# Kernel optimization log

Hardware: AMD Instinct MI355X
Metric: run time of the kernel (lower is better)

The kernel has to match this reference:

```python
import jax, jax.numpy as jnp
import numpy as np

DIM = 256; CTX_DIM = 256; K = 7; SK = 5; NH = 4  # num_heads*2
HD = DIM // NH; SCALE = HD ** -0.5
H = 64; W = 64; HC = 56; WC = 56
LN_EPS = 1e-6; BN_EPS = 1e-5


def make_bias_idx(k, h, w):
    # Faithful port of ContMix.generate_idx + apply_rpb index construction.
    rs = 2 * k - 1
    idx_h = np.arange(k); idx_w = np.arange(k)
    idx_k = (idx_h[:, None] * rs + idx_w).reshape(-1)
    rep_h = np.ones(k, np.int64); rep_h[k // 2] = h - (k - 1)
    rep_w = np.ones(k, np.int64); rep_w[k // 2] = w - (k - 1)
    bias_hw = np.repeat(idx_h, rep_h)[:, None] * rs + np.repeat(idx_w, rep_w)  # (h, w)
    bias_idx = (bias_hw[..., None] + idx_k).reshape(-1, k * k)                 # (h*w, k^2)
    return jnp.asarray(bias_idx[::-1].copy())  # torch.flip along dim 0


def window_idx(n, k):
    # NATTEN-style clamped neighborhood window starts.
    s = np.clip(np.arange(n) - k // 2, 0, n - k)
    return jnp.asarray(s[:, None] + np.arange(k))  # (n, k)


BIDX1 = make_bias_idx(SK, H, W)
BIDX2 = make_bias_idx(K, H, W)
IDXI_S = window_idx(H, SK); IDXJ_S = window_idx(W, SK)
IDXI_L = window_idx(H, K);  IDXJ_L = window_idx(W, K)


def ln2d(x, g, b):
    # LayerNorm over channel dim per spatial location, x: (B, C, H, W)
    mu = x.mean(1, keepdims=True)
    var = ((x - mu) ** 2).mean(1, keepdims=True)
    return (x - mu) * jax.lax.rsqrt(var + LN_EPS) * g[None, :, None, None] + b[None, :, None, None]


def conv1x1(x, Wt):
    return jnp.einsum('oc,bchw->bohw', Wt, x)


def apply_rpb(attn, rpb, bias_idx, h, w):
    g = rpb.shape[0]
    r = rpb.reshape(g, -1)[:, bias_idx]  # (g, h*w, k^2)
    return attn + r.reshape(1, g, h, w, -1)


def na2d_av(attn, value, k, idx_i, idx_j):
    # attn: (B, G, H, W, k^2), value: (B, G, H, W, C)
    B, G, h, w, _ = attn.shape
    v = value[:, :, idx_i]        # (B, G, H, k, W, C)
    v = v[:, :, :, :, idx_j]      # (B, G, H, k, W, k, C)
    a = attn.reshape(B, G, h, w, k, k)
    return jnp.einsum('bghwpq,bghpwqc->bghwc', a, v)


def contmix_forward(x, ctx, Wq, gq, bq, Wk, gk, bk, Wproj, rpb1, rpb2, Wdy, bn_g, bn_b):
    B = x.shape[0]
    q = ln2d(conv1x1(x, Wq), gq, bq) * SCALE                       # (B, DIM, H, W)
    # AdaptiveAvgPool2d(7) on 56x56 -> exact 8x8 bins
    kctx = ctx.reshape(B, CTX_DIM, 7, HC // 7, 7, WC // 7).mean((3, 5))
    kf = ln2d(conv1x1(kctx, Wk), gk, bk)                            # (B, DIM, 7, 7)
    q = q.reshape(B, NH, HD, H * W)
    kf = kf.reshape(B, NH, HD, 49)
    wgt = jnp.einsum('bgcn,bgcl->bgnl', q, kf)                      # (B, 4, HW, 49)
    wgt = jnp.einsum('ml,bgnl->bgnm', Wproj, wgt)                   # (B, 4, HW, 74)
    wgt = wgt.reshape(B, NH, H, W, SK * SK + K * K)
    attn1 = wgt[:, :NH // 2, :, :, :SK * SK]                        # group1, 25
    attn2 = wgt[:, NH // 2:, :, :, SK * SK:]                        # group2, 49
    attn1 = jax.nn.softmax(apply_rpb(attn1, rpb1, BIDX1, H, W), -1)
    attn2 = jax.nn.softmax(apply_rpb(attn2, rpb2, BIDX2, H, W), -1)
    # 'b (m g c) h w -> m b g h w c', m=2, g=2
    v = x.reshape(B, 2, NH // 2, HD, H, W).transpose(1, 0, 2, 4, 5, 3)
    x1 = na2d_av(attn1, v[0], SK, IDXI_S, IDXJ_S)                   # (B, 2, H, W, HD)
    x2 = na2d_av(attn2, v[1], K, IDXI_L, IDXJ_L)
    out = jnp.concatenate([x1, x2], axis=1)                         # (B, 4, H, W, HD)
    out = out.transpose(0, 1, 4, 2, 3).reshape(B, DIM, H, W)
    out = conv1x1(out, Wdy)
    # BatchNorm2d in eval mode: running_mean=0, running_var=1
    out = out * (bn_g * jax.lax.rsqrt(jnp.float32(1.0) + BN_EPS))[None, :, None, None] + bn_b[None, :, None, None]
    return out


def setup_inputs() -> dict:
    key = jax.random.key(0)
    ks = jax.random.split(key, 10)
    d = {}
    d['x'] = jax.random.normal(ks[0], (4, DIM, H, W), jnp.float32)
    d['ctx'] = jax.random.normal(ks[1], (4, CTX_DIM, HC, WC), jnp.float32)
    d['Wq'] = jax.random.normal(ks[2], (DIM, DIM), jnp.float32) * 0.02
    d['gq'] = jnp.ones((DIM,), jnp.float32)
    d['bq'] = jnp.zeros((DIM,), jnp.float32)
    d['Wk'] = jax.random.normal(ks[3], (DIM, CTX_DIM), jnp.float32) * 0.02
    d['gk'] = jnp.ones((DIM,), jnp.float32)
    d['bk'] = jnp.zeros((DIM,), jnp.float32)
    d['Wproj'] = jax.random.normal(ks[4], (SK * SK + K * K, 49), jnp.float32) * 0.1
    d['rpb1'] = jax.random.normal(ks[5], (NH // 2, 2 * SK - 1, 2 * SK - 1), jnp.float32) * 0.02
    d['rpb2'] = jax.random.normal(ks[6], (NH // 2, 2 * K - 1, 2 * K - 1), jnp.float32) * 0.02
    d['Wdy'] = jax.random.normal(ks[7], (DIM, DIM), jnp.float32) * 0.02
    d['bn_g'] = jnp.ones((DIM,), jnp.float32)
    d['bn_b'] = jnp.zeros((DIM,), jnp.float32)
    return d


def reference(x, ctx, Wq, gq, bq, Wk, gk, bk, Wproj, rpb1, rpb2, Wdy, bn_g, bn_b):
    return contmix_forward(x, ctx, Wq, gq, bq, Wk, gk, bk, Wproj, rpb1, rpb2, Wdy, bn_g, bn_b)
```

## Files before the change

kernel.cpp:

```cpp
#include <hip/hip_runtime.h>

#define DEV __device__ __forceinline__

typedef __bf16 bf16x8 __attribute__((ext_vector_type(8)));
typedef __bf16 bf16x4 __attribute__((ext_vector_type(4)));
typedef float floatx4 __attribute__((ext_vector_type(4)));

__global__ __launch_bounds__(256)
void prep_kernel(const float* __restrict__ Wq, const float* __restrict__ Wdy,
                 const float* __restrict__ ctx, const float* __restrict__ x,
                 __bf16* __restrict__ wqb, __bf16* __restrict__ wdyb,
                 float* __restrict__ kctx, __bf16* __restrict__ xt) {
  __shared__ float tile[64][65];
  int bid = blockIdx.x, t = threadIdx.x;
  if (bid < 256) {
    int i = bid * 256 + t;
    wqb[i]  = (__bf16)Wq[i];
    wdyb[i] = (__bf16)Wdy[i];
  } else if (bid < 512) {
    int bc = (bid - 256) * 4 + (t >> 6);
    const float* src = ctx + (size_t)bc * (56 * 56);
    int w = t & 63;
#pragma unroll
    for (int pi = 0; pi < 7; ++pi) {
      float s = 0.f;
      if (w < 56) {
#pragma unroll
        for (int di = 0; di < 8; ++di) s += src[(pi * 8 + di) * 56 + w];
      }
      s += __shfl_down(s, 4);
      s += __shfl_down(s, 2);
      s += __shfl_down(s, 1);
      if (w < 56 && (w & 7) == 0)
        kctx[(size_t)bc * 49 + pi * 7 + (w >> 3)] = s * (1.f / 64.f);
    }
  } else {
    int idx = bid - 512;
    int b = idx >> 8, c0 = ((idx >> 6) & 3) * 64, n0 = (idx & 63) * 64;
    int lane = t & 63, rg = t >> 6;
    const float* src = x + ((size_t)b * 256 + c0) * 4096 + n0;
    for (int i = rg; i < 64; i += 4) tile[i][lane] = src[(size_t)i * 4096 + lane];
    __syncthreads();
    __bf16* dst = xt + ((size_t)b * 4096 + n0) * 256 + c0;
    for (int i = rg; i < 64; i += 4) dst[(size_t)i * 256 + lane] = (__bf16)tile[lane][i];
  }
}

__global__ __launch_bounds__(256)
void kf_ln_kernel(const float* __restrict__ kctx, const float* __restrict__ Wk,
                  const float* __restrict__ gk, const float* __restrict__ bk,
                  float* __restrict__ kf) {
  int b = blockIdx.x / 49, l = blockIdx.x % 49;
  __shared__ float xs[256];
  __shared__ float r1[4], r2[4];
  int o = threadIdx.x;
  xs[o] = kctx[((size_t)b * 256 + o) * 49 + l];
  __syncthreads();
  const float* wrow = Wk + (size_t)o * 256;
  float acc = 0.f;
#pragma unroll 8
  for (int c = 0; c < 256; c += 4) {
    float4 wv = *(const float4*)(wrow + c);
    acc += wv.x * xs[c] + wv.y * xs[c + 1] + wv.z * xs[c + 2] + wv.w * xs[c + 3];
  }
  float s1 = acc, s2 = acc * acc;
#pragma unroll
  for (int off = 32; off > 0; off >>= 1) {
    s1 += __shfl_down(s1, off);
    s2 += __shfl_down(s2, off);
  }
  int wv_ = o >> 6, ln = o & 63;
  if (ln == 0) { r1[wv_] = s1; r2[wv_] = s2; }
  __syncthreads();
  float mu  = (r1[0] + r1[1] + r1[2] + r1[3]) * (1.f / 256.f);
  float var = (r2[0] + r2[1] + r2[2] + r2[3]) * (1.f / 256.f) - mu * mu;
  float rstd = rsqrtf(var + 1e-6f);
  kf[((size_t)b * 256 + o) * 49 + l] = (acc - mu) * rstd * gk[o] + bk[o];
}

__global__ __launch_bounds__(256)
void kfp_kernel(const float* __restrict__ kf, const float* __restrict__ Wproj,
                __bf16* __restrict__ kfpT) {
  int bg = blockIdx.x; int b = bg >> 2, g = bg & 3;
  int m0 = blockIdx.y * 16;
  __shared__ float kfs[64][50];
  __shared__ float wps[16][50];
  int t = threadIdx.x;
  for (int i = t; i < 64 * 49; i += 256) {
    int d = i / 49, l = i % 49;
    kfs[d][l] = kf[((size_t)b * 256 + g * 64 + d) * 49 + l];
  }
  for (int i = t; i < 16 * 49; i += 256) {
    int m = i / 49, l = i % 49;
    wps[m][l] = (m0 + m < 74) ? Wproj[(m0 + m) * 49 + l] : 0.f;
  }
  __syncthreads();
  for (int i = t; i < 64 * 16; i += 256) {
    int d = i >> 4, m = i & 15;
    float s = 0.f;
    if (m0 + m < 74) {
#pragma unroll 7
      for (int l = 0; l < 49; ++l) s += kfs[d][l] * wps[m][l];
    }
    kfpT[(size_t)bg * 5120 + (m0 + m) * 64 + d] = (__bf16)s;
  }
}

DEV int rep_idx(int p, int kc, int t1, int sub) {
  return p < kc ? p : (p < t1 ? kc : p - sub);
}

template <int KK>
DEV void softmax_write(const float* wms, const float* rpb_s, __bf16* __restrict__ attnL,
                       int bg, int n_glob, int row) {
  constexpr int CNT = KK * KK;
  constexpr int RS  = 2 * KK - 1;
  constexpr int KC  = KK / 2;
  constexpr int T1  = KC + (64 - KK + 1);
  constexpr int SUB = 64 - KK;
  constexpr int MLO = (KK == 5) ? 0 : 25;
  constexpr int PW  = (KK == 5) ? 32 : 56;
  int h = n_glob >> 6, w = n_glob & 63;
  int rh = rep_idx(63 - h, KC, T1, SUB);
  int rw = rep_idx(63 - w, KC, T1, SUB);
  float vals[CNT];
  float mx = -1e30f;
#pragma unroll
  for (int m = 0; m < CNT; ++m) {
    int ki = m / KK, kj = m % KK;
    float v = wms[row * 81 + MLO + m] + rpb_s[(rh + ki) * RS + rw + kj];
    vals[m] = v; mx = fmaxf(mx, v);
  }
  float ssum = 0.f;
#pragma unroll
  for (int m = 0; m < CNT; ++m) { float e = __expf(vals[m] - mx); vals[m] = e; ssum += e; }
  float inv = 1.f / ssum;
  __bf16 hv[PW];
#pragma unroll
  for (int m = 0; m < PW; ++m) hv[m] = (__bf16)(m < CNT ? vals[m] * inv : 0.f);
  __bf16* ap = attnL + ((size_t)bg * 4096 + n_glob) * 56;
#pragma unroll
  for (int i = 0; i < PW / 8; ++i) *(bf16x8*)(ap + i * 8) = *(bf16x8*)&hv[i * 8];
}

__global__ __launch_bounds__(512, 1)
void qattn_kernel(const __bf16* __restrict__ Wb, const __bf16* __restrict__ XT,
                  const __bf16* __restrict__ kfpT,
                  const float* __restrict__ gq, const float* __restrict__ bq,
                  const float* __restrict__ rpb1, const float* __restrict__ rpb2,
                  __bf16* __restrict__ attnL) {
  __shared__ float wms[256 * 81];
  __shared__ float rpb_s[500];
  __shared__ float gqs[256], bqs[256];
  __shared__ float red_s[4][64], red_q[4][64];
  __shared__ float st_mu[64], st_rs[64];
  __bf16* As  = (__bf16*)wms;
  __bf16* Bs  = (__bf16*)wms + 256 * 72;
  __bf16* Aat = (__bf16*)wms;

  int b  = blockIdx.z;
  int n0 = blockIdx.x * 64;
  int t  = threadIdx.x;
  int lane = t & 63, wv = t >> 6;
  int oq = wv & 3, nh = wv >> 2;
  int col = lane & 15, quad = lane >> 4;

  if (t < 256) {
    gqs[t] = gq[t] * 0.125f;
    bqs[t] = bq[t] * 0.125f;
  }
  for (int i = t; i < 162; i += 512) rpb_s[i] = rpb1[i];
  for (int i = t; i < 338; i += 512) rpb_s[162 + i] = rpb2[i];

  floatx4 acc[4][2];
#pragma unroll
  for (int i = 0; i < 4; ++i)
#pragma unroll
    for (int j = 0; j < 2; ++j) acc[i][j] = {0.f, 0.f, 0.f, 0.f};

  int rowA = t >> 1, kA = (t & 1) * 32;
  int rowB = t >> 3, kB = (t & 7) * 8;
  const __bf16* wp = Wb + (size_t)rowA * 256 + kA;
  const __bf16* xp = XT + ((size_t)b * 4096 + n0 + rowB) * 256 + kB;
  bf16x8 ra0 = *(const bf16x8*)wp;
  bf16x8 ra1 = *(const bf16x8*)(wp + 8);
  bf16x8 ra2 = *(const bf16x8*)(wp + 16);
  bf16x8 ra3 = *(const bf16x8*)(wp + 24);
  bf16x8 rb  = *(const bf16x8*)xp;

  for (int c0 = 0; c0 < 256; c0 += 64) {
    *(bf16x8*)&As[rowA * 72 + kA]      = ra0;
    *(bf16x8*)&As[rowA * 72 + kA + 8]  = ra1;
    *(bf16x8*)&As[rowA * 72 + kA + 16] = ra2;
    *(bf16x8*)&As[rowA * 72 + kA + 24] = ra3;
    *(bf16x8*)&Bs[rowB * 72 + kB]      = rb;
    __syncthreads();
    if (c0 + 64 < 256) {
      ra0 = *(const bf16x8*)(wp + c0 + 64);
      ra1 = *(const bf16x8*)(wp + c0 + 72);
      ra2 = *(const bf16x8*)(wp + c0 + 80);
      ra3 = *(const bf16x8*)(wp + c0 + 88);
      rb  = *(const bf16x8*)(xp + c0 + 64);
    }
    bf16x8 fa[2][4], fb[2][2];
#pragma unroll
    for (int ks = 0; ks < 2; ++ks) {
#pragma unroll
      for (int i = 0; i < 4; ++i)
        fa[ks][i] = *(const bf16x8*)&As[(oq * 64 + i * 16 + col) * 72 + ks * 32 + quad * 8];
#pragma unroll
      for (int j = 0; j < 2; ++j)
        fb[ks][j] = *(const bf16x8*)&Bs[(nh * 32 + j * 16 + col) * 72 + ks * 32 + quad * 8];
    }
#pragma unroll
    for (int ks = 0; ks < 2; ++ks)
#pragma unroll
      for (int i = 0; i < 4; ++i)
#pragma unroll
        for (int j = 0; j < 2; ++j)
          acc[i][j] = __builtin_amdgcn_mfma_f32_16x16x32_bf16(fa[ks][i], fb[ks][j], acc[i][j], 0, 0, 0);
    __syncthreads();
  }

#pragma unroll
  for (int j = 0; j < 2; ++j) {
    float s = 0.f, q = 0.f;
#pragma unroll
    for (int i = 0; i < 4; ++i)
#pragma unroll
      for (int r = 0; r < 4; ++r) { float v = acc[i][j][r]; s += v; q += v * v; }
    s += __shfl_xor(s, 16); s += __shfl_xor(s, 32);
    q += __shfl_xor(q, 16); q += __shfl_xor(q, 32);
    if (quad == 0) {
      red_s[oq][nh * 32 + j * 16 + col] = s;
      red_q[oq][nh * 32 + j * 16 + col] = q;
    }
  }
  __syncthreads();
  if (t < 64) {
    float s = red_s[0][t] + red_s[1][t] + red_s[2][t] + red_s[3][t];
    float q = red_q[0][t] + red_q[1][t] + red_q[2][t] + red_q[3][t];
    float mu  = s * (1.f / 256.f);
    float var = q * (1.f / 256.f) - mu * mu;
    st_mu[t] = mu;
    st_rs[t] = rsqrtf(var + 1e-6f);
  }
  __syncthreads();

#pragma unroll
  for (int j = 0; j < 2; ++j) {
    int n_loc = nh * 32 + j * 16 + col;
    float mu = st_mu[n_loc], rs = st_rs[n_loc];
#pragma unroll
    for (int i = 0; i < 4; ++i) {
      __bf16 pk[4];
#pragma unroll
      for (int r = 0; r < 4; ++r) {
        int o = oq * 64 + i * 16 + quad * 4 + r;
        pk[r] = (__bf16)((acc[i][j][r] - mu) * rs * gqs[o] + bqs[o]);
      }
      *(bf16x4*)&Aat[((size_t)(oq * 64 + n_loc)) * 72 + i * 16 + quad * 4] = *(bf16x4*)pk;
    }
  }
  __syncthreads();

  bf16x8 fa2[2][2], fb2[2][5];
  const __bf16* kp = kfpT + (size_t)(b * 4 + oq) * 5120;
#pragma unroll
  for (int ks = 0; ks < 2; ++ks) {
#pragma unroll
    for (int a = 0; a < 2; ++a)
      fa2[ks][a] = *(const bf16x8*)&Aat[((size_t)(oq * 64 + nh * 32 + a * 16 + col)) * 72 + ks * 32 + quad * 8];
#pragma unroll
    for (int nt = 0; nt < 5; ++nt)
      fb2[ks][nt] = *(const bf16x8*)&kp[(nt * 16 + col) * 64 + ks * 32 + quad * 8];
  }
  floatx4 acc2[2][5];
#pragma unroll
  for (int a = 0; a < 2; ++a)
#pragma unroll
    for (int nt = 0; nt < 5; ++nt) acc2[a][nt] = {0.f, 0.f, 0.f, 0.f};
#pragma unroll
  for (int ks = 0; ks < 2; ++ks)
#pragma unroll
    for (int a = 0; a < 2; ++a)
#pragma unroll
      for (int nt = 0; nt < 5; ++nt)
        acc2[a][nt] = __builtin_amdgcn_mfma_f32_16x16x32_bf16(fa2[ks][a], fb2[ks][nt], acc2[a][nt], 0, 0, 0);
  __syncthreads();

#pragma unroll
  for (int a = 0; a < 2; ++a)
#pragma unroll
    for (int nt = 0; nt < 5; ++nt)
#pragma unroll
      for (int r = 0; r < 4; ++r)
        wms[(oq * 64 + nh * 32 + a * 16 + quad * 4 + r) * 81 + nt * 16 + col] = acc2[a][nt][r];
  __syncthreads();

  if (t < 256) {
    int g2 = t >> 6;
    int n_glob = n0 + (t & 63);
    int bg = b * 4 + g2;
    if (g2 < 2) softmax_write<5>(wms, rpb_s + g2 * 81,              attnL, bg, n_glob, t);
    else        softmax_write<7>(wms, rpb_s + 162 + (g2 - 2) * 169, attnL, bg, n_glob, t);
  }
}

template <int MODE>
__global__ __launch_bounds__(256, 2)
void conv_mfma_kernel(const __bf16* __restrict__ Wb, const __bf16* __restrict__ Xin,
                      void* __restrict__ Yout, float* __restrict__ stats,
                      const float* __restrict__ bn_g, const float* __restrict__ bn_b) {
  int b  = blockIdx.z;
  int n0 = blockIdx.x * 64;
  int o0 = blockIdx.y * 128;
  __shared__ __bf16 As[128 * 72];
  __shared__ __bf16 Bs[64 * 72];
  int t = threadIdx.x;
  int lane = t & 63, wv = t >> 6;
  int mq = (wv & 1) * 64, nq = (wv >> 1) * 32;
  int col = lane & 15, quad = lane >> 4;
  floatx4 acc[4][2];
#pragma unroll
  for (int i = 0; i < 4; ++i)
#pragma unroll
    for (int j = 0; j < 2; ++j) acc[i][j] = {0.f, 0.f, 0.f, 0.f};
  int sm = t >> 1, skA = (t & 1) * 32;
  int snB = t >> 2, kB16 = (t & 3) * 16;
  const __bf16* wp = Wb + (size_t)(o0 + sm) * 256 + skA;
  auto xaddr = [&](int c0) -> const __bf16* {
    if (MODE == 0) {
      return Xin + ((size_t)b * 4096 + n0 + snB) * 256 + c0 + kB16;
    } else {
      int c = c0 + kB16, g = c >> 6, c64 = c & 63;
      return Xin + (((size_t)(b * 4 + g)) * 4096 + n0 + snB) * 64 + c64;
    }
  };
  bf16x8 wa0 = *(const bf16x8*)wp;
  bf16x8 wa1 = *(const bf16x8*)(wp + 8);
  bf16x8 wa2 = *(const bf16x8*)(wp + 16);
  bf16x8 wa3 = *(const bf16x8*)(wp + 24);
  const __bf16* x0 = xaddr(0);
  bf16x8 xb0 = *(const bf16x8*)x0;
  bf16x8 xb1 = *(const bf16x8*)(x0 + 8);
  for (int c0 = 0; c0 < 256; c0 += 64) {
    *(bf16x8*)&As[sm * 72 + skA]      = wa0;
    *(bf16x8*)&As[sm * 72 + skA + 8]  = wa1;
    *(bf16x8*)&As[sm * 72 + skA + 16] = wa2;
    *(bf16x8*)&As[sm * 72 + skA + 24] = wa3;
    *(bf16x8*)&Bs[snB * 72 + kB16]     = xb0;
    *(bf16x8*)&Bs[snB * 72 + kB16 + 8] = xb1;
    __syncthreads();
    if (c0 + 64 < 256) {
      wa0 = *(const bf16x8*)(wp + c0 + 64);
      wa1 = *(const bf16x8*)(wp + c0 + 72);
      wa2 = *(const bf16x8*)(wp + c0 + 80);
      wa3 = *(const bf16x8*)(wp + c0 + 88);
      const __bf16* xn = xaddr(c0 + 64);
      xb0 = *(const bf16x8*)xn;
      xb1 = *(const bf16x8*)(xn + 8);
    }
    bf16x8 fa[2][4], fb[2][2];
#pragma unroll
    for (int ks = 0; ks < 2; ++ks) {
#pragma unroll
      for (int i = 0; i < 4; ++i)
        fa[ks][i] = *(const bf16x8*)&As[(mq + i * 16 + col) * 72 + ks * 32 + quad * 8];
#pragma unroll
      for (int j = 0; j < 2; ++j)
        fb[ks][j] = *(const bf16x8*)&Bs[(nq + j * 16 + col) * 72 + ks * 32 + quad * 8];
    }
#pragma unroll
    for (int ks = 0; ks < 2; ++ks)
#pragma unroll
      for (int i = 0; i < 4; ++i)
#pragma unroll
        for (int j = 0; j < 2; ++j)
          acc[i][j] = __builtin_amdgcn_mfma_f32_16x16x32_bf16(fa[ks][i], fb[ks][j], acc[i][j], 0, 0, 0);
    __syncthreads();
  }
  {
    float* Yf = (float*)Yout + (size_t)b * 256 * 4096;
#pragma unroll
    for (int i = 0; i < 4; ++i) {
#pragma unroll
      for (int r = 0; r < 4; ++r) {
        int o = o0 + mq + i * 16 + quad * 4 + r;
        float scale = bn_g[o] * 0.9999950000374997f;
        float shift = bn_b[o];
        float* yrow = Yf + (size_t)o * 4096 + n0 + nq + col;
#pragma unroll
        for (int j = 0; j < 2; ++j) yrow[j * 16] = acc[i][j][r] * scale + shift;
      }
    }
  }
}

template <int KK>
DEV void na2d_body8(const __bf16* __restrict__ attnL, const __bf16* __restrict__ XT,
                    __bf16* __restrict__ midT, float* xs, int bg, int h0, int chalf, int t) {
  constexpr int CNT = KK * KK, KC = KK / 2, SMAX = 64 - KK;
  constexpr int ROWS = KK + 7;
  constexpr int PW = (KK == 5) ? 32 : 56;
  int b = bg >> 2, g = bg & 3;
  int si0 = min(max(h0 - KC, 0), SMAX);
  {
    int sn = t & 63, sc8 = (t >> 6) & 3, rh = t >> 8;
    const __bf16* src = XT + ((size_t)b * 4096 + sn) * 256 + g * 64 + chalf * 32 + sc8 * 8;
    for (int r = rh; r < ROWS; r += 2) {
      int gr = min(si0 + r, 63);
      bf16x8 v = *(const bf16x8*)(src + (size_t)gr * 64 * 256);
      float f[8];
#pragma unroll
      for (int e = 0; e < 8; ++e) f[e] = (float)v[e];
      float* d = &xs[(r * 64 + sn) * 36 + sc8 * 8];
      *(float4*)d       = *(float4*)&f[0];
      *(float4*)(d + 4) = *(float4*)&f[4];
    }
  }
  __syncthreads();
  int w = t & 63, cg = (t >> 6) & 3, hh = t >> 8;
  int sj = min(max(w - KC, 0), SMAX);
#pragma unroll
  for (int h4 = 0; h4 < 4; ++h4) {
    int h = h0 + hh * 4 + h4;
    int base = min(max(h - KC, 0), SMAX) - si0;
    bf16x8 avh[PW / 8];
    const __bf16* ap = attnL + ((size_t)bg * 4096 + h * 64 + w) * 56;
#pragma unroll
    for (int i = 0; i < PW / 8; ++i) avh[i] = *(const bf16x8*)(ap + i * 8);
    float av[CNT];
#pragma unroll
    for (int m = 0; m < CNT; ++m) av[m] = (float)avh[m / 8][m % 8];
    float acc[8] = {};
#pragma unroll
    for (int p = 0; p < KK; ++p) {
      const float* xr = &xs[((base + p) * 64 + sj) * 36 + cg * 8];
#pragma unroll
      for (int q = 0; q < KK; ++q) {
        float4 v0 = *(const float4*)(xr + q * 36);
        float4 v1 = *(const float4*)(xr + q * 36 + 4);
        float a = av[p * KK + q];
        acc[0] += a * v0.x; acc[1] += a * v0.y; acc[2] += a * v0.z; acc[3] += a * v0.w;
        acc[4] += a * v1.x; acc[5] += a * v1.y; acc[6] += a * v1.z; acc[7] += a * v1.w;
      }
    }
    __bf16 hv[8];
#pragma unroll
    for (int e = 0; e < 8; ++e) hv[e] = (__bf16)acc[e];
    *(bf16x8*)&midT[((size_t)bg * 4096 + h * 64 + w) * 64 + chalf * 32 + cg * 8] = *(bf16x8*)hv;
  }
}

__global__ __launch_bounds__(512, 1)
void na2d_kernel(const __bf16* __restrict__ attnL, const __bf16* __restrict__ XT,
                 __bf16* __restrict__ midT) {
  __shared__ float xs[14 * 64 * 36];
  int bg = blockIdx.x, h0 = blockIdx.y * 8, chalf = blockIdx.z, t = threadIdx.x;
  if ((bg & 3) < 2) na2d_body8<5>(attnL, XT, midT, xs, bg, h0, chalf, t);
  else              na2d_body8<7>(attnL, XT, midT, xs, bg, h0, chalf, t);
}

extern "C" void kernel_launch(void* const* d_in, const int* in_sizes, int n_in,
                              void* d_out, int out_size, void* d_ws, size_t ws_size,
                              hipStream_t stream) {
  const float* x     = (const float*)d_in[0];
  const float* ctx   = (const float*)d_in[1];
  const float* Wq    = (const float*)d_in[2];
  const float* gq    = (const float*)d_in[3];
  const float* bq    = (const float*)d_in[4];
  const float* Wk    = (const float*)d_in[5];
  const float* gk    = (const float*)d_in[6];
  const float* bk    = (const float*)d_in[7];
  const float* Wproj = (const float*)d_in[8];
  const float* rpb1  = (const float*)d_in[9];
  const float* rpb2  = (const float*)d_in[10];
  const float* Wdy   = (const float*)d_in[11];
  const float* bn_g  = (const float*)d_in[12];
  const float* bn_b  = (const float*)d_in[13];
  float* out = (float*)d_out;

  float* ws     = (float*)d_ws;
  float* kctx   = ws;
  float* kf     = kctx + 50176;
  __bf16* attnL = (__bf16*)(kf + 50176);
  __bf16* wqb   = attnL + 3670016;
  __bf16* wdyb  = wqb + 65536;
  __bf16* kfpT  = wdyb + 65536;
  __bf16* XT    = kfpT + 81920;
  __bf16* midT  = XT + 4194304;

  prep_kernel<<<dim3(1536), dim3(256), 0, stream>>>(Wq, Wdy, ctx, x, wqb, wdyb, kctx, XT);
  kf_ln_kernel<<<dim3(196), dim3(256), 0, stream>>>(kctx, Wk, gk, bk, kf);
  kfp_kernel<<<dim3(16, 5), dim3(256), 0, stream>>>(kf, Wproj, kfpT);
  qattn_kernel<<<dim3(64, 1, 4), dim3(512), 0, stream>>>(wqb, XT, kfpT, gq, bq, rpb1, rpb2, attnL);
  na2d_kernel<<<dim3(16, 8, 2), dim3(512), 0, stream>>>(attnL, XT, midT);
  conv_mfma_kernel<1><<<dim3(64, 2, 4), dim3(256), 0, stream>>>(wdyb, midT, out, nullptr, bn_g, bn_b);
}
```

Measured before the change: 154.2 us.

## Double-buffer LDS tiles in GEMM kernels and vectorize prep transposes

The qattn and conv GEMM main loops now ping-pong between two LDS buffers. The next tile is stored while the current tile's fragments are in flight, which leaves one barrier per k-step instead of two. The prep kernel converts weights with float4 loads and bf16x4 stores, and transposes x with float4 reads and bf16x8 writes. LDS use grows (qattn smem goes to about 92KB), which may limit occupancy. The padded transpose tile could still see bank conflicts on the strided reads.

```diff
diff --git a/kernel.cpp b/kernel.cpp
--- a/kernel.cpp
+++ b/kernel.cpp
@@ -11,14 +11,18 @@
                  const float* __restrict__ ctx, const float* __restrict__ x,
                  __bf16* __restrict__ wqb, __bf16* __restrict__ wdyb,
                  float* __restrict__ kctx, __bf16* __restrict__ xt) {
-  __shared__ float tile[64][65];
+  __shared__ float tile[64][67];
   int bid = blockIdx.x, t = threadIdx.x;
-  if (bid < 256) {
-    int i = bid * 256 + t;
-    wqb[i]  = (__bf16)Wq[i];
-    wdyb[i] = (__bf16)Wdy[i];
-  } else if (bid < 512) {
-    int bc = (bid - 256) * 4 + (t >> 6);
+  if (bid < 64) {
+    int i = bid * 1024 + t * 4;
+    float4 a = *(const float4*)(Wq + i);
+    float4 d = *(const float4*)(Wdy + i);
+    __bf16 ha[4] = {(__bf16)a.x, (__bf16)a.y, (__bf16)a.z, (__bf16)a.w};
+    __bf16 hd[4] = {(__bf16)d.x, (__bf16)d.y, (__bf16)d.z, (__bf16)d.w};
+    *(bf16x4*)&wqb[i]  = *(bf16x4*)ha;
+    *(bf16x4*)&wdyb[i] = *(bf16x4*)hd;
+  } else if (bid < 320) {
+    int bc = (bid - 64) * 4 + (t >> 6);
     const float* src = ctx + (size_t)bc * (56 * 56);
     int w = t & 63;
 #pragma unroll
@@ -35,14 +39,30 @@
         kctx[(size_t)bc * 49 + pi * 7 + (w >> 3)] = s * (1.f / 64.f);
     }
   } else {
-    int idx = bid - 512;
+    int idx = bid - 320;
     int b = idx >> 8, c0 = ((idx >> 6) & 3) * 64, n0 = (idx & 63) * 64;
-    int lane = t & 63, rg = t >> 6;
     const float* src = x + ((size_t)b * 256 + c0) * 4096 + n0;
-    for (int i = rg; i < 64; i += 4) tile[i][lane] = src[(size_t)i * 4096 + lane];
+    int cr = t >> 4, nl = (t & 15) * 4;
+#pragma unroll
+    for (int p = 0; p < 4; ++p) {
+      int c = p * 16 + cr;
+      float4 v = *(const float4*)(src + (size_t)c * 4096 + nl);
+      tile[c][nl]     = v.x;
+      tile[c][nl + 1] = v.y;
+      tile[c][nl + 2] = v.z;
+      tile[c][nl + 3] = v.w;
+    }
     __syncthreads();
     __bf16* dst = xt + ((size_t)b * 4096 + n0) * 256 + c0;
-    for (int i = rg; i < 64; i += 4) dst[(size_t)i * 256 + lane] = (__bf16)tile[lane][i];
+    int c8 = (t & 7) * 8;
+#pragma unroll
+    for (int p = 0; p < 2; ++p) {
+      int n = p * 32 + (t >> 3);
+      __bf16 hv[8];
+#pragma unroll
+      for (int e = 0; e < 8; ++e) hv[e] = (__bf16)tile[c8 + e][n];
+      *(bf16x8*)(dst + (size_t)n * 256 + c8) = *(bf16x8*)hv;
+    }
   }
 }
 
@@ -149,14 +169,15 @@
                   const float* __restrict__ gq, const float* __restrict__ bq,
                   const float* __restrict__ rpb1, const float* __restrict__ rpb2,
                   __bf16* __restrict__ attnL) {
-  __shared__ float wms[256 * 81];
+  __shared__ __align__(16) float smem[23040];
   __shared__ float rpb_s[500];
   __shared__ float gqs[256], bqs[256];
   __shared__ float red_s[4][64], red_q[4][64];
   __shared__ float st_mu[64], st_rs[64];
-  __bf16* As  = (__bf16*)wms;
-  __bf16* Bs  = (__bf16*)wms + 256 * 72;
-  __bf16* Aat = (__bf16*)wms;
+  float* wms  = smem;
+  __bf16* Aat = (__bf16*)smem;
+  __bf16* Ab0 = (__bf16*)smem;
+  __bf16* Ab1 = (__bf16*)smem + 23040;
 
   int b  = blockIdx.z;
   int n0 = blockIdx.x * 64;
@@ -187,30 +208,51 @@
   bf16x8 ra2 = *(const bf16x8*)(wp + 16);
   bf16x8 ra3 = *(const bf16x8*)(wp + 24);
   bf16x8 rb  = *(const bf16x8*)xp;
-
-  for (int c0 = 0; c0 < 256; c0 += 64) {
-    *(bf16x8*)&As[rowA * 72 + kA]      = ra0;
-    *(bf16x8*)&As[rowA * 72 + kA + 8]  = ra1;
-    *(bf16x8*)&As[rowA * 72 + kA + 16] = ra2;
-    *(bf16x8*)&As[rowA * 72 + kA + 24] = ra3;
-    *(bf16x8*)&Bs[rowB * 72 + kB]      = rb;
-    __syncthreads();
-    if (c0 + 64 < 256) {
-      ra0 = *(const bf16x8*)(wp + c0 + 64);
-      ra1 = *(const bf16x8*)(wp + c0 + 72);
-      ra2 = *(const bf16x8*)(wp + c0 + 80);
-      ra3 = *(const bf16x8*)(wp + c0 + 88);
-      rb  = *(const bf16x8*)(xp + c0 + 64);
-    }
+  {
+    __bf16* A = Ab0; __bf16* B = Ab0 + 18432;
+    *(bf16x8*)&A[rowA * 72 + kA]      = ra0;
+    *(bf16x8*)&A[rowA * 72 + kA + 8]  = ra1;
+    *(bf16x8*)&A[rowA * 72 + kA + 16] = ra2;
+    *(bf16x8*)&A[rowA * 72 + kA + 24] = ra3;
+    *(bf16x8*)&B[rowB * 72 + kB]      = rb;
+  }
+  ra0 = *(const bf16x8*)(wp + 64);
+  ra1 = *(const bf16x8*)(wp + 72);
+  ra2 = *(const bf16x8*)(wp + 80);
+  ra3 = *(const bf16x8*)(wp + 88);
+  rb  = *(const bf16x8*)(xp + 64);
+  __syncthreads();
+
+#pragma unroll
+  for (int k = 0; k < 4; ++k) {
+    __bf16* A = (k & 1) ? Ab1 : Ab0;
+    __bf16* B = A + 18432;
     bf16x8 fa[2][4], fb[2][2];
 #pragma unroll
     for (int ks = 0; ks < 2; ++ks) {
 #pragma unroll
       for (int i = 0; i < 4; ++i)
-        fa[ks][i] = *(const bf16x8*)&As[(oq * 64 + i * 16 + col) * 72 + ks * 32 + quad * 8];
+        fa[ks][i] = *(const bf16x8*)&A[(oq * 64 + i * 16 + col) * 72 + ks * 32 + quad * 8];
 #pragma unroll
       for (int j = 0; j < 2; ++j)
-        fb[ks][j] = *(const bf16x8*)&Bs[(nh * 32 + j * 16 + col) * 72 + ks * 32 + quad * 8];
+        fb[ks][j] = *(const bf16x8*)&B[(nh * 32 + j * 16 + col) * 72 + ks * 32 + quad * 8];
+    }
+    if (k < 3) {
+      __bf16* An = (k & 1) ? Ab0 : Ab1;
+      __bf16* Bn = An + 18432;
+      *(bf16x8*)&An[rowA * 72 + kA]      = ra0;
+      *(bf16x8*)&An[rowA * 72 + kA + 8]  = ra1;
+      *(bf16x8*)&An[rowA * 72 + kA + 16] = ra2;
+      *(bf16x8*)&An[rowA * 72 + kA + 24] = ra3;
+      *(bf16x8*)&Bn[rowB * 72 + kB]      = rb;
+    }
+    if (k < 2) {
+      int cn = (k + 2) * 64;
+      ra0 = *(const bf16x8*)(wp + cn);
+      ra1 = *(const bf16x8*)(wp + cn + 8);
+      ra2 = *(const bf16x8*)(wp + cn + 16);
+      ra3 = *(const bf16x8*)(wp + cn + 24);
+      rb  = *(const bf16x8*)(xp + cn);
     }
 #pragma unroll
     for (int ks = 0; ks < 2; ++ks)
@@ -219,7 +261,7 @@
 #pragma unroll
         for (int j = 0; j < 2; ++j)
           acc[i][j] = __builtin_amdgcn_mfma_f32_16x16x32_bf16(fa[ks][i], fb[ks][j], acc[i][j], 0, 0, 0);
-    __syncthreads();
+    if (k < 3) __syncthreads();
   }
 
 #pragma unroll
@@ -315,8 +357,9 @@
   int b  = blockIdx.z;
   int n0 = blockIdx.x * 64;
   int o0 = blockIdx.y * 128;
-  __shared__ __bf16 As[128 * 72];
-  __shared__ __bf16 Bs[64 * 72];
+  __shared__ __align__(16) __bf16 smem[2 * 13824];
+  __bf16* Ab0 = smem;
+  __bf16* Ab1 = smem + 13824;
   int t = threadIdx.x;
   int lane = t & 63, wv = t >> 6;
   int mq = (wv & 1) * 64, nq = (wv >> 1) * 32;
@@ -344,33 +387,60 @@
   const __bf16* x0 = xaddr(0);
   bf16x8 xb0 = *(const bf16x8*)x0;
   bf16x8 xb1 = *(const bf16x8*)(x0 + 8);
-  for (int c0 = 0; c0 < 256; c0 += 64) {
-    *(bf16x8*)&As[sm * 72 + skA]      = wa0;
-    *(bf16x8*)&As[sm * 72 + skA + 8]  = wa1;
-    *(bf16x8*)&As[sm * 72 + skA + 16] = wa2;
-    *(bf16x8*)&As[sm * 72 + skA + 24] = wa3;
-    *(bf16x8*)&Bs[snB * 72 + kB16]     = xb0;
-    *(bf16x8*)&Bs[snB * 72 + kB16 + 8] = xb1;
-    __syncthreads();
-    if (c0 + 64 < 256) {
-      wa0 = *(const bf16x8*)(wp + c0 + 64);
-      wa1 = *(const bf16x8*)(wp + c0 + 72);
-      wa2 = *(const bf16x8*)(wp + c0 + 80);
-      wa3 = *(const bf16x8*)(wp + c0 + 88);
-      const __bf16* xn = xaddr(c0 + 64);
+  {
+    __bf16* A = Ab0; __bf16* B = Ab0 + 9216;
+    *(bf16x8*)&A[sm * 72 + skA]      = wa0;
+    *(bf16x8*)&A[sm * 72 + skA + 8]  = wa1;
+    *(bf16x8*)&A[sm * 72 + skA + 16] = wa2;
+    *(bf16x8*)&A[sm * 72 + skA + 24] = wa3;
+    *(bf16x8*)&B[snB * 72 + kB16]     = xb0;
+    *(bf16x8*)&B[snB * 72 + kB16 + 8] = xb1;
+  }
+  wa0 = *(const bf16x8*)(wp + 64);
+  wa1 = *(const bf16x8*)(wp + 72);
+  wa2 = *(const bf16x8*)(wp + 80);
+  wa3 = *(const bf16x8*)(wp + 88);
+  {
+    const __bf16* xn = xaddr(64);
+    xb0 = *(const bf16x8*)xn;
+    xb1 = *(const bf16x8*)(xn + 8);
+  }
+  __syncthreads();
+
+#pragma unroll
+  for (int k = 0; k < 4; ++k) {
+    __bf16* A = (k & 1) ? Ab1 : Ab0;
+    __bf16* B = A + 9216;
+    bf16x8 fa[2][4], fb[2][2];
+#pragma unroll
+    for (int ks = 0; ks < 2; ++ks) {
+#pragma unroll
+      for (int i = 0; i < 4; ++i)
+        fa[ks][i] = *(const bf16x8*)&A[(mq + i * 16 + col) * 72 + ks * 32 + quad * 8];
+#pragma unroll
+      for (int j = 0; j < 2; ++j)
+        fb[ks][j] = *(const bf16x8*)&B[(nq + j * 16 + col) * 72 + ks * 32 + quad * 8];
+    }
+    if (k < 3) {
+      __bf16* An = (k & 1) ? Ab0 : Ab1;
+      __bf16* Bn = An + 9216;
+      *(bf16x8*)&An[sm * 72 + skA]      = wa0;
+      *(bf16x8*)&An[sm * 72 + skA + 8]  = wa1;
+      *(bf16x8*)&An[sm * 72 + skA + 16] = wa2;
+      *(bf16x8*)&An[sm * 72 + skA + 24] = wa3;
+      *(bf16x8*)&Bn[snB * 72 + kB16]     = xb0;
+      *(bf16x8*)&Bn[snB * 72 + kB16 + 8] = xb1;
+    }
+    if (k < 2) {
+      int cn = (k + 2) * 64;
+      wa0 = *(const bf16x8*)(wp + cn);
+      wa1 = *(const bf16x8*)(wp + cn + 8);
+      wa2 = *(const bf16x8*)(wp + cn + 16);
+      wa3 = *(const bf16x8*)(wp + cn + 24);
+      const __bf16* xn = xaddr(cn);
       xb0 = *(const bf16x8*)xn;
       xb1 = *(const bf16x8*)(xn + 8);
     }
-    bf16x8 fa[2][4], fb[2][2];
-#pragma unroll
-    for (int ks = 0; ks < 2; ++ks) {
-#pragma unroll
-      for (int i = 0; i < 4; ++i)
-        fa[ks][i] = *(const bf16x8*)&As[(mq + i * 16 + col) * 72 + ks * 32 + quad * 8];
-#pragma unroll
-      for (int j = 0; j < 2; ++j)
-        fb[ks][j] = *(const bf16x8*)&Bs[(nq + j * 16 + col) * 72 + ks * 32 + quad * 8];
-    }
 #pragma unroll
     for (int ks = 0; ks < 2; ++ks)
 #pragma unroll
@@ -378,7 +448,7 @@
 #pragma unroll
         for (int j = 0; j < 2; ++j)
           acc[i][j] = __builtin_amdgcn_mfma_f32_16x16x32_bf16(fa[ks][i], fb[ks][j], acc[i][j], 0, 0, 0);
-    __syncthreads();
+    if (k < 3) __syncthreads();
   }
   {
     float* Yf = (float*)Yout + (size_t)b * 256 * 4096;
@@ -491,7 +561,7 @@
   __bf16* XT    = kfpT + 81920;
   __bf16* midT  = XT + 4194304;
 
-  prep_kernel<<<dim3(1536), dim3(256), 0, stream>>>(Wq, Wdy, ctx, x, wqb, wdyb, kctx, XT);
+  prep_kernel<<<dim3(1344), dim3(256), 0, stream>>>(Wq, Wdy, ctx, x, wqb, wdyb, kctx, XT);
   kf_ln_kernel<<<dim3(196), dim3(256), 0, stream>>>(kctx, Wk, gk, bk, kf);
   kfp_kernel<<<dim3(16, 5), dim3(256), 0, stream>>>(kf, Wproj, kfpT);
   qattn_kernel<<<dim3(64, 1, 4), dim3(512), 0, stream>>>(wqb, XT, kfpT, gq, bq, rpb1, rpb2, attnL);
```

Measured after the change: 153.6 us. Within noise of the previous version (-0.4%).
